# Performance work log

Hardware: AMD Instinct MI355X
Metric: run time of the kernel (lower is better)

## Reference

```python
import jax, jax.numpy as jnp
import numpy as np

B, T, I, H = 64, 1024, 256, 256

def setup_inputs() -> dict:
    key = jax.random.key(0)
    ks = jax.random.split(key, 14)
    s_in = 1.0 / np.sqrt(I)
    s_h = 1.0 / np.sqrt(H)
    return {
        "inputs": jax.random.normal(ks[0], (B, T, I), jnp.float32),
        "h0": jax.random.normal(ks[1], (B, H), jnp.float32),
        "Wz": jax.random.normal(ks[2], (I, H), jnp.float32) * s_in,
        "Wr": jax.random.normal(ks[3], (I, H), jnp.float32) * s_in,
        "Wh": jax.random.normal(ks[4], (I, H), jnp.float32) * s_in,
        "bz": jax.random.normal(ks[5], (H,), jnp.float32) * s_in,
        "br": jax.random.normal(ks[6], (H,), jnp.float32) * s_in,
        "bh": jax.random.normal(ks[7], (H,), jnp.float32) * s_in,
        "Uz": jax.random.normal(ks[8], (H, H), jnp.float32) * s_h,
        "Ur": jax.random.normal(ks[9], (H, H), jnp.float32) * s_h,
        "Uh": jax.random.normal(ks[10], (H, H), jnp.float32) * s_h,
        "cz": jax.random.normal(ks[11], (H,), jnp.float32) * s_h,
        "cr": jax.random.normal(ks[12], (H,), jnp.float32) * s_h,
        "ch": jax.random.normal(ks[13], (H,), jnp.float32) * s_h,
    }


def reference(inputs, h0, Wz, Wr, Wh, bz, br, bh, Uz, Ur, Uh, cz, cr, ch):
    # Precompute all input projections in one pass (same math as per-step linears).
    # inputs: [B,T,I] -> x_*: [T,B,H] (time-major for scan)
    xz = jnp.einsum('bti,ih->tbh', inputs, Wz) + bz
    xr = jnp.einsum('bti,ih->tbh', inputs, Wr) + br
    xh = jnp.einsum('bti,ih->tbh', inputs, Wh) + bh

    def step(h, x_t):
        x_z, x_r, x_h = x_t
        z = jax.nn.sigmoid(x_z + h @ Uz + cz)
        r = jax.nn.sigmoid(x_r + h @ Ur + cr)
        h_hat = jnp.tanh(x_h + r * (h @ Uh + ch))
        h_new = z * h + (1.0 - z) * h_hat
        return h_new, h_new

    h_last, outs = jax.lax.scan(step, h0, (xz, xr, xh))
    outputs = jnp.transpose(outs, (1, 0, 2))  # [B,T,H] (batch_first)
    return outputs, h_last
```

## Files before the change

kernel.cpp:

```cpp
#include <hip/hip_runtime.h>
#include <stdint.h>


typedef float  f32x4 __attribute__((ext_vector_type(4)));
typedef short  s16x8 __attribute__((ext_vector_type(8)));
typedef unsigned short u16;

#define MFMA_BF16(a, b, c) __builtin_amdgcn_mfma_f32_16x16x32_bf16((a), (b), (c), 0, 0, 0)
#define L2E 1.4426950408889634f

static __device__ __forceinline__ u16 f2bf(float f) {
  uint32_t u = __float_as_uint(f);
  u += 0x7FFFu + ((u >> 16) & 1u);
  return (u16)(u >> 16);
}
static __device__ __forceinline__ uint32_t cvt_pk_bf16(float lo, float hi) {
  uint32_t r;
  asm("v_cvt_pk_bf16_f32 %0, %1, %2" : "=v"(r) : "v"(lo), "v"(hi));
  return r;
}
static __device__ __forceinline__ float fast_exp2(float x) {
#if __has_builtin(__builtin_amdgcn_exp2f)
  return __builtin_amdgcn_exp2f(x);
#else
  return exp2f(x);
#endif
}
static __device__ __forceinline__ float fast_rcp(float x) {
#if __has_builtin(__builtin_amdgcn_rcpf)
  return __builtin_amdgcn_rcpf(x);
#else
  return 1.0f / x;
#endif
}
static __device__ __forceinline__ float tanh_(float x) {
  float ax = fabsf(x);
  float e  = fast_exp2(-2.885390081777927f * ax);
  float r  = (1.0f - e) * fast_rcp(1.0f + e);
  return x < 0.0f ? -r : r;
}

#define WS_BIAS_OFF  786432
#define WS_X_OFF     (1u << 20)


__global__ __launch_bounds__(256) void k_prep(
    const float* __restrict__ Wz, const float* __restrict__ Wr, const float* __restrict__ Wh,
    const float* __restrict__ Uz, const float* __restrict__ Ur, const float* __restrict__ Uh,
    const float* __restrict__ bz, const float* __restrict__ br, const float* __restrict__ bh,
    const float* __restrict__ cz, const float* __restrict__ cr, const float* __restrict__ ch,
    u16* __restrict__ wfrag, float* __restrict__ wbias)
{
  if (blockIdx.x == 192) {
    int c = threadIdx.x;
    wbias[c]       = bz[c] + cz[c];
    wbias[256 + c] = br[c] + cr[c];
    wbias[512 + c] = bh[c];
    return;
  }
  int tid = blockIdx.x * 256 + threadIdx.x;
  int mat = tid >> 13;
  int kk  = (tid >> 10) & 7;
  int n   = (tid >> 6) & 15;
  int l   = tid & 63;
  const float* M = (mat == 0) ? Wz : (mat == 1) ? Wr : (mat == 2) ? Wh
                 : (mat == 3) ? Uz : (mat == 4) ? Ur : Uh;
  int col   = n * 16 + (l & 15);
  int kbase = kk * 32 + (l >> 4) * 8;
  uint32_t d[4];
#pragma unroll
  for (int p = 0; p < 4; ++p) {
    u16 lo = f2bf(M[(kbase + 2 * p    ) * 256 + col]);
    u16 hi = f2bf(M[(kbase + 2 * p + 1) * 256 + col]);
    d[p] = (uint32_t)lo | ((uint32_t)hi << 16);
  }
  uint32_t* dst = (uint32_t*)(wfrag + ((size_t)mat * 65536 + (size_t)((kk * 16 + n) * 64 + l) * 8));
  dst[0] = d[0]; dst[1] = d[1]; dst[2] = d[2]; dst[3] = d[3];
}

__global__ __launch_bounds__(256) void k_proj(
    const float* __restrict__ X, const u16* __restrict__ wfrag,
    const float* __restrict__ wbias, u16* __restrict__ xout)
{
  const int t   = blockIdx.x;
  const int tid = threadIdx.x;
  const int l   = tid & 63;
  const int w   = tid >> 6;

  const float* xrow = X + ((size_t)(w * 16 + (l & 15)) * 1024 + t) * 256 + (l >> 4) * 8;
  s16x8 af[8];
#pragma unroll
  for (int kk = 0; kk < 8; ++kk) {
    f32x4 a0 = *(const f32x4*)(xrow + kk * 32);
    f32x4 a1 = *(const f32x4*)(xrow + kk * 32 + 4);
    union { uint32_t d[4]; s16x8 v; } U;
    U.d[0] = cvt_pk_bf16(a0[0], a0[1]);
    U.d[1] = cvt_pk_bf16(a0[2], a0[3]);
    U.d[2] = cvt_pk_bf16(a1[0], a1[1]);
    U.d[3] = cvt_pk_bf16(a1[2], a1[3]);
    af[kk] = U.v;
  }

  const s16x8* WB = (const s16x8*)wfrag;
  const int g = w;
#pragma unroll
  for (int m = 0; m < 3; ++m) {
    f32x4 acc[16];
#pragma unroll
    for (int n = 0; n < 16; ++n) acc[n] = 0.0f;
#pragma unroll
    for (int kk = 0; kk < 8; ++kk) {
#pragma unroll
      for (int n = 0; n < 16; ++n) {
        s16x8 bf = WB[(size_t)m * 8192 + (kk * 16 + n) * 64 + l];
        acc[n] = MFMA_BF16(af[kk], bf, acc[n]);
      }
    }
    const float scale = (m < 2) ? -L2E : 1.0f;
#pragma unroll
    for (int n = 0; n < 16; ++n) {
      int col = n * 16 + (l & 15);
      float b = wbias[m * 256 + col];
      float v0 = (acc[n][0] + b) * scale;
      float v1 = (acc[n][1] + b) * scale;
      float v2 = (acc[n][2] + b) * scale;
      float v3 = (acc[n][3] + b) * scale;
      uint32_t w0 = cvt_pk_bf16(v0, v1);
      uint32_t w1 = cvt_pk_bf16(v2, v3);
      size_t idx = ((((size_t)m * 1024 + t) * 4 + g) * 16 + n) * 64 + l;
      ((uint64_t*)xout)[idx] = (uint64_t)w0 | ((uint64_t)w1 << 32);
    }
  }
}

__global__ __launch_bounds__(512, 2) void k_rnn(
    const u16* __restrict__ wfrag, const u16* __restrict__ xin,
    const float* __restrict__ h0, const float* __restrict__ ch,
    float* __restrict__ out)
{
  __shared__ __align__(16) u16 hb[2][512];

  const int blk = blockIdx.x;
  const int tid = threadIdx.x;
  const int l   = tid & 63;
  const int w   = tid >> 6;
  const int col16 = l & 15;
  const int nt    = (l >> 4) & 1;
  const int rg    = l >> 5;
  const int cgate = w * 32 + nt * 16 + col16;
  const int b     = 2 * blk + rg;

  const s16x8* WB = (const s16x8*)wfrag;

  s16x8 BZ[2][8], BR[2][8], BH[2][8];
#pragma unroll
  for (int q = 0; q < 2; ++q) {
    int n = 2 * w + q;
#pragma unroll
    for (int kk = 0; kk < 8; ++kk) {
      BZ[q][kk] = WB[(size_t)3 * 8192 + (kk * 16 + n) * 64 + l];
      BR[q][kk] = WB[(size_t)4 * 8192 + (kk * 16 + n) * 64 + l];
      BH[q][kk] = WB[(size_t)5 * 8192 + (kk * 16 + n) * 64 + l];
    }
  }

  const float chv = ch[cgate];
  float hp = h0[(size_t)b * 256 + cgate];

  hb[0][tid] = f2bf(h0[(size_t)(2 * blk + (tid >> 8)) * 256 + (tid & 255)]);
  __syncthreads();

  char* hbbase = (char*)&hb[0][0];
  const int rd_off = (col16 & 1) * 512 + (l >> 4) * 16;
  const int wb_off = rg * 512 + cgate * 2;

  const uint32_t* x32 = (const uint32_t*)xin;
  const int n_ = 2 * w + nt;
  uint32_t xo = (uint32_t)(((blk >> 3) * 16 + n_) * 64 + ((blk & 7) >> 1) * 16 + col16) * 2u
              + (uint32_t)(blk & 1);
  const uint32_t XM = 8388608u;
  uint32_t oo = (uint32_t)b * 262144u + (uint32_t)cgate;

  uint32_t nx0 = x32[xo], nx1 = x32[xo + XM], nx2 = x32[xo + 2u * XM];

  int hoff = 0;
  const uint32_t xsel = rg ? 0xffff0000u : 0u;

  for (int t = 0; t < 1024; ++t) {
    uint32_t cx0 = nx0, cx1 = nx1, cx2 = nx2;
    xo += (t < 1023) ? 8192u : 0u;
    nx0 = x32[xo]; nx1 = x32[xo + XM]; nx2 = x32[xo + 2u * XM];

    const char* rdp = hbbase + hoff + rd_off;

    f32x4 az0 = 0.0f, az1 = 0.0f, ar0 = 0.0f, ar1 = 0.0f, ah0 = 0.0f, ah1 = 0.0f;
#pragma unroll
    for (int kk = 0; kk < 8; ++kk) {
      s16x8 a_ = *(const s16x8*)(rdp + kk * 64);
      az0 = MFMA_BF16(a_, BZ[0][kk], az0);
      ar0 = MFMA_BF16(a_, BR[0][kk], ar0);
      ah0 = MFMA_BF16(a_, BH[0][kk], ah0);
      az1 = MFMA_BF16(a_, BZ[1][kk], az1);
      ar1 = MFMA_BF16(a_, BR[1][kk], ar1);
      ah1 = MFMA_BF16(a_, BH[1][kk], ah1);
    }

    float vz = rg ? (nt ? az1[1] : az0[1]) : (nt ? az1[0] : az0[0]);
    float vr = rg ? (nt ? ar1[1] : ar0[1]) : (nt ? ar1[0] : ar0[0]);
    float vh = rg ? (nt ? ah1[1] : ah0[1]) : (nt ? ah1[0] : ah0[0]);

    float xz = __uint_as_float(rg ? (cx0 & xsel) : (cx0 << 16));
    float xr = __uint_as_float(rg ? (cx1 & xsel) : (cx1 << 16));
    float xh = __uint_as_float(rg ? (cx2 & xsel) : (cx2 << 16));

    float z_  = fast_rcp(1.0f + fast_exp2(fmaf(vz, -L2E, xz)));
    float rgt = fast_rcp(1.0f + fast_exp2(fmaf(vr, -L2E, xr)));
    float th  = tanh_(fmaf(rgt, vh + chv, xh));
    float hn  = fmaf(z_, hp - th, th);
    hp = hn;

    *(u16*)(hbbase + (hoff ^ 1024) + wb_off) = f2bf(hn);
    out[oo] = hn;
    oo += 256u;

    hoff ^= 1024;
    asm volatile("s_waitcnt lgkmcnt(0)" ::: "memory");
    __builtin_amdgcn_s_barrier();
  }

  out[16777216u + (uint32_t)b * 256u + (uint32_t)cgate] = hp;
}

extern "C" void kernel_launch(void* const* d_in, const int* in_sizes, int n_in,
                              void* d_out, int out_size, void* d_ws, size_t ws_size,
                              hipStream_t stream) {
  const float* X  = (const float*)d_in[0];
  const float* h0 = (const float*)d_in[1];
  const float* Wz = (const float*)d_in[2];
  const float* Wr = (const float*)d_in[3];
  const float* Wh = (const float*)d_in[4];
  const float* bz = (const float*)d_in[5];
  const float* br = (const float*)d_in[6];
  const float* bh = (const float*)d_in[7];
  const float* Uz = (const float*)d_in[8];
  const float* Ur = (const float*)d_in[9];
  const float* Uh = (const float*)d_in[10];
  const float* cz = (const float*)d_in[11];
  const float* cr = (const float*)d_in[12];
  const float* ch = (const float*)d_in[13];

  char*  ws    = (char*)d_ws;
  u16*   wfrag = (u16*)ws;
  float* wbias = (float*)(ws + WS_BIAS_OFF);
  u16*   xbuf  = (u16*)(ws + WS_X_OFF);
  float* out   = (float*)d_out;

  k_prep<<<193, 256, 0, stream>>>(Wz, Wr, Wh, Uz, Ur, Uh, bz, br, bh, cz, cr, ch,
                                  wfrag, wbias);
  k_proj<<<1024, 256, 0, stream>>>(X, wfrag, wbias, xbuf);
  k_rnn<<<32, 512, 0, stream>>>(wfrag, xbuf, h0, ch, out);
}
```

Baseline: 1.138 ms.

## Retile projection GEMM over 8 waves and stage recurrent gate MFMAs

The input-projection kernel now runs 512 threads per block. Each wave computes a 2x4 tile of 16x16 outputs, so every B fragment loaded from memory is reused across two row tiles, where before each wave covered all 16 column tiles of one row tile. In the recurrent kernel, all eight h fragments are loaded from shared memory up front, and the z, r and h gate MFMAs are issued as separate groups so each gate's sigmoid can overlap with the remaining matrix work. The bf16 conversion of the new hidden state now uses the hardware packed-convert instruction, and the extra live registers may increase register pressure.

```diff
diff --git a/kernel.cpp b/kernel.cpp
--- a/kernel.cpp
+++ b/kernel.cpp
@@ -78,7 +78,7 @@
   dst[0] = d[0]; dst[1] = d[1]; dst[2] = d[2]; dst[3] = d[3];
 }
 
-__global__ __launch_bounds__(256) void k_proj(
+__global__ __launch_bounds__(512) void k_proj(
     const float* __restrict__ X, const u16* __restrict__ wfrag,
     const float* __restrict__ wbias, u16* __restrict__ xout)
 {
@@ -86,49 +86,61 @@
   const int tid = threadIdx.x;
   const int l   = tid & 63;
   const int w   = tid >> 6;
-
-  const float* xrow = X + ((size_t)(w * 16 + (l & 15)) * 1024 + t) * 256 + (l >> 4) * 8;
-  s16x8 af[8];
-#pragma unroll
-  for (int kk = 0; kk < 8; ++kk) {
-    f32x4 a0 = *(const f32x4*)(xrow + kk * 32);
-    f32x4 a1 = *(const f32x4*)(xrow + kk * 32 + 4);
-    union { uint32_t d[4]; s16x8 v; } U;
-    U.d[0] = cvt_pk_bf16(a0[0], a0[1]);
-    U.d[1] = cvt_pk_bf16(a0[2], a0[3]);
-    U.d[2] = cvt_pk_bf16(a1[0], a1[1]);
-    U.d[3] = cvt_pk_bf16(a1[2], a1[3]);
-    af[kk] = U.v;
+  const int p   = w >> 2;
+  const int q   = w & 3;
+
+  s16x8 af[2][8];
+#pragma unroll
+  for (int mti = 0; mti < 2; ++mti) {
+    const float* xrow = X + ((size_t)((2 * p + mti) * 16 + (l & 15)) * 1024 + t) * 256
+                        + (l >> 4) * 8;
+#pragma unroll
+    for (int kk = 0; kk < 8; ++kk) {
+      f32x4 a0 = *(const f32x4*)(xrow + kk * 32);
+      f32x4 a1 = *(const f32x4*)(xrow + kk * 32 + 4);
+      union { uint32_t d[4]; s16x8 v; } U;
+      U.d[0] = cvt_pk_bf16(a0[0], a0[1]);
+      U.d[1] = cvt_pk_bf16(a0[2], a0[3]);
+      U.d[2] = cvt_pk_bf16(a1[0], a1[1]);
+      U.d[3] = cvt_pk_bf16(a1[2], a1[3]);
+      af[mti][kk] = U.v;
+    }
   }
 
   const s16x8* WB = (const s16x8*)wfrag;
-  const int g = w;
 #pragma unroll
   for (int m = 0; m < 3; ++m) {
-    f32x4 acc[16];
-#pragma unroll
-    for (int n = 0; n < 16; ++n) acc[n] = 0.0f;
-#pragma unroll
-    for (int kk = 0; kk < 8; ++kk) {
-#pragma unroll
-      for (int n = 0; n < 16; ++n) {
-        s16x8 bf = WB[(size_t)m * 8192 + (kk * 16 + n) * 64 + l];
-        acc[n] = MFMA_BF16(af[kk], bf, acc[n]);
+    f32x4 acc[2][4];
+#pragma unroll
+    for (int mti = 0; mti < 2; ++mti)
+#pragma unroll
+      for (int nti = 0; nti < 4; ++nti) acc[mti][nti] = 0.0f;
+#pragma unroll
+    for (int kk = 0; kk < 8; ++kk) {
+#pragma unroll
+      for (int nti = 0; nti < 4; ++nti) {
+        s16x8 bf = WB[(size_t)m * 8192 + (kk * 16 + 4 * q + nti) * 64 + l];
+        acc[0][nti] = MFMA_BF16(af[0][kk], bf, acc[0][nti]);
+        acc[1][nti] = MFMA_BF16(af[1][kk], bf, acc[1][nti]);
       }
     }
     const float scale = (m < 2) ? -L2E : 1.0f;
 #pragma unroll
-    for (int n = 0; n < 16; ++n) {
-      int col = n * 16 + (l & 15);
-      float b = wbias[m * 256 + col];
-      float v0 = (acc[n][0] + b) * scale;
-      float v1 = (acc[n][1] + b) * scale;
-      float v2 = (acc[n][2] + b) * scale;
-      float v3 = (acc[n][3] + b) * scale;
-      uint32_t w0 = cvt_pk_bf16(v0, v1);
-      uint32_t w1 = cvt_pk_bf16(v2, v3);
-      size_t idx = ((((size_t)m * 1024 + t) * 4 + g) * 16 + n) * 64 + l;
-      ((uint64_t*)xout)[idx] = (uint64_t)w0 | ((uint64_t)w1 << 32);
+    for (int mti = 0; mti < 2; ++mti) {
+#pragma unroll
+      for (int nti = 0; nti < 4; ++nti) {
+        int n   = 4 * q + nti;
+        int col = n * 16 + (l & 15);
+        float b = wbias[m * 256 + col];
+        float v0 = (acc[mti][nti][0] + b) * scale;
+        float v1 = (acc[mti][nti][1] + b) * scale;
+        float v2 = (acc[mti][nti][2] + b) * scale;
+        float v3 = (acc[mti][nti][3] + b) * scale;
+        uint32_t w0 = cvt_pk_bf16(v0, v1);
+        uint32_t w1 = cvt_pk_bf16(v2, v3);
+        size_t idx = ((((size_t)m * 1024 + t) * 4 + (2 * p + mti)) * 16 + n) * 64 + l;
+        ((uint64_t*)xout)[idx] = (uint64_t)w0 | ((uint64_t)w1 << 32);
+      }
     }
   }
 }
@@ -193,33 +205,45 @@
 
     const char* rdp = hbbase + hoff + rd_off;
 
-    f32x4 az0 = 0.0f, az1 = 0.0f, ar0 = 0.0f, ar1 = 0.0f, ah0 = 0.0f, ah1 = 0.0f;
-#pragma unroll
-    for (int kk = 0; kk < 8; ++kk) {
-      s16x8 a_ = *(const s16x8*)(rdp + kk * 64);
-      az0 = MFMA_BF16(a_, BZ[0][kk], az0);
-      ar0 = MFMA_BF16(a_, BR[0][kk], ar0);
-      ah0 = MFMA_BF16(a_, BH[0][kk], ah0);
-      az1 = MFMA_BF16(a_, BZ[1][kk], az1);
-      ar1 = MFMA_BF16(a_, BR[1][kk], ar1);
-      ah1 = MFMA_BF16(a_, BH[1][kk], ah1);
-    }
-
+    s16x8 a_[8];
+#pragma unroll
+    for (int kk = 0; kk < 8; ++kk) a_[kk] = *(const s16x8*)(rdp + kk * 64);
+
+    f32x4 az0 = 0.0f, az1 = 0.0f;
+#pragma unroll
+    for (int kk = 0; kk < 8; ++kk) {
+      az0 = MFMA_BF16(a_[kk], BZ[0][kk], az0);
+      az1 = MFMA_BF16(a_[kk], BZ[1][kk], az1);
+    }
     float vz = rg ? (nt ? az1[1] : az0[1]) : (nt ? az1[0] : az0[0]);
-    float vr = rg ? (nt ? ar1[1] : ar0[1]) : (nt ? ar1[0] : ar0[0]);
+    float xz = __uint_as_float(rg ? (cx0 & xsel) : (cx0 << 16));
+    float z_ = fast_rcp(1.0f + fast_exp2(fmaf(vz, -L2E, xz)));
+
+    f32x4 ar0 = 0.0f, ar1 = 0.0f;
+#pragma unroll
+    for (int kk = 0; kk < 8; ++kk) {
+      ar0 = MFMA_BF16(a_[kk], BR[0][kk], ar0);
+      ar1 = MFMA_BF16(a_[kk], BR[1][kk], ar1);
+    }
+    float vr  = rg ? (nt ? ar1[1] : ar0[1]) : (nt ? ar1[0] : ar0[0]);
+    float xr  = __uint_as_float(rg ? (cx1 & xsel) : (cx1 << 16));
+    float rgt = fast_rcp(1.0f + fast_exp2(fmaf(vr, -L2E, xr)));
+
+    f32x4 ah0 = 0.0f, ah1 = 0.0f;
+#pragma unroll
+    for (int kk = 0; kk < 8; ++kk) {
+      ah0 = MFMA_BF16(a_[kk], BH[0][kk], ah0);
+      ah1 = MFMA_BF16(a_[kk], BH[1][kk], ah1);
+    }
     float vh = rg ? (nt ? ah1[1] : ah0[1]) : (nt ? ah1[0] : ah0[0]);
-
-    float xz = __uint_as_float(rg ? (cx0 & xsel) : (cx0 << 16));
-    float xr = __uint_as_float(rg ? (cx1 & xsel) : (cx1 << 16));
     float xh = __uint_as_float(rg ? (cx2 & xsel) : (cx2 << 16));
 
-    float z_  = fast_rcp(1.0f + fast_exp2(fmaf(vz, -L2E, xz)));
-    float rgt = fast_rcp(1.0f + fast_exp2(fmaf(vr, -L2E, xr)));
-    float th  = tanh_(fmaf(rgt, vh + chv, xh));
-    float hn  = fmaf(z_, hp - th, th);
+    float th = tanh_(fmaf(rgt, vh + chv, xh));
+    float hn = fmaf(z_, hp - th, th);
     hp = hn;
 
-    *(u16*)(hbbase + (hoff ^ 1024) + wb_off) = f2bf(hn);
+    uint32_t pk = cvt_pk_bf16(hn, hn);
+    *(u16*)(hbbase + (hoff ^ 1024) + wb_off) = (u16)pk;
     out[oo] = hn;
     oo += 256u;
 
@@ -257,6 +281,6 @@
 
   k_prep<<<193, 256, 0, stream>>>(Wz, Wr, Wh, Uz, Ur, Uh, bz, br, bh, cz, cr, ch,
                                   wfrag, wbias);
-  k_proj<<<1024, 256, 0, stream>>>(X, wfrag, wbias, xbuf);
+  k_proj<<<1024, 512, 0, stream>>>(X, wfrag, wbias, xbuf);
   k_rnn<<<32, 512, 0, stream>>>(wfrag, xbuf, h0, ch, out);
 }
```

Result: faster. 1.001 ms (-12.0%).
